# Kernel optimization log

Measured on AMD Instinct MI355X. Metric: run time of the kernel, lower is better.

## Reference

```python
import jax, jax.numpy as jnp
import numpy as np
import math

B, S, HID = 2, 2048, 1536
H, HD = 12, 128           # num_heads, head_dim
LAT = HID // 8            # latent_dim = 192
ROT = HD // 2             # 64, rotary applied to this half-size subspace


def _make_rotary(seq_len, dim=ROT, base=10000.0):
    # LlamaRotaryEmbedding: inv_freq over dim/2 freqs, emb = cat(sin, cos) -> [1,1,S,dim]
    inv_freq = 1.0 / (base ** (np.arange(0, dim, 2, dtype=np.float32) / dim))
    pos = np.arange(seq_len, dtype=np.float32)
    sincos = np.einsum('i,j->ij', pos, inv_freq)  # [S, dim/2]
    emb = np.concatenate([np.sin(sincos), np.cos(sincos)], axis=-1)  # [S, dim]
    return jnp.asarray(emb)[None, None, :, :]


def setup_inputs() -> dict:
    key = jax.random.key(0)
    ks = jax.random.split(key, 10)
    sd = 0.02
    return {
        'hidden_states': jax.random.normal(ks[0], (B, S, HID), jnp.float32),
        'rotary_emb': _make_rotary(S),
        'W_kv_d':  jax.random.normal(ks[1], (HID, LAT), jnp.float32) * sd,
        'W_q_d':   jax.random.normal(ks[2], (HID, LAT), jnp.float32) * sd,
        'W_k_u':   jax.random.normal(ks[3], (LAT, H * ROT), jnp.float32) * sd,
        'W_q_u':   jax.random.normal(ks[4], (LAT, H * ROT), jnp.float32) * sd,
        'W_v_u':   jax.random.normal(ks[5], (LAT, H * HD), jnp.float32) * sd,
        'W_rope_k': jax.random.normal(ks[6], (HID, HID // 2), jnp.float32) * sd,
        'W_rope_q': jax.random.normal(ks[7], (LAT, HID // 2), jnp.float32) * sd,
        'W_o':     jax.random.normal(ks[8], (HID, HID), jnp.float32) * sd,
    }


def _apply_rope(x, emb):
    # x: [B,S,H,ROT]; emb: [1,1,S,ROT] (cat of sin,cos, each ROT/2)
    half = ROT // 2
    x1, x2 = x[..., :half], x[..., half:]
    sin = emb[..., :half].transpose(0, 2, 1, 3)  # -> [1,S,1,half] to broadcast over heads
    cos = emb[..., half:].transpose(0, 2, 1, 3)
    return jnp.concatenate([x1 * cos - x2 * sin, x1 * sin + x2 * cos], axis=-1)


def reference(hidden_states, rotary_emb, W_kv_d, W_q_d, W_k_u, W_q_u, W_v_u,
              W_rope_k, W_rope_q, W_o):
    b, s, _ = hidden_states.shape
    kv_d = hidden_states @ W_kv_d                       # [B,S,LAT]
    q_d = hidden_states @ W_q_d                         # [B,S,LAT]
    k_c = (kv_d @ W_k_u).reshape(b, s, H, ROT)          # content half of K
    q_c = (q_d @ W_q_u).reshape(b, s, H, ROT)
    v = (kv_d @ W_v_u).reshape(b, s, H, HD)
    k_r = (hidden_states @ W_rope_k).reshape(b, s, H, ROT)
    q_r = (q_d @ W_rope_q).reshape(b, s, H, ROT)
    k_r = _apply_rope(k_r, rotary_emb)
    q_r = _apply_rope(q_r, rotary_emb)
    k = jnp.concatenate([k_c, k_r], axis=-1)            # [B,S,H,HD]
    q = jnp.concatenate([q_c, q_r], axis=-1)

    scores = jnp.einsum('bqhd,bkhd->bhqk', q, k) / math.sqrt(HD)
    causal = jnp.tril(jnp.ones((s, s), dtype=bool))
    scores = jnp.where(causal[None, None], scores, jnp.float32(-1e9))
    probs = jax.nn.softmax(scores, axis=-1)
    attn = jnp.einsum('bhqk,bkhd->bqhd', probs, v).reshape(b, s, HID)
    return attn @ W_o
```

## Files before the change

### kernel.cpp

```cpp
#include <hip/hip_runtime.h>
#include <hip/hip_bf16.h>

#define B_ 2
#define S_ 2048
#define HID_ 1536
#define H_ 12
#define HD_ 128
#define LAT_ 192
#define ROT_ 64
#define M_ (B_*S_)
#define NTILE_ (B_*H_*(S_/64))

#define SC2F 0.12752869f

typedef __hip_bfloat16 bf16;

using short8  = __attribute__((ext_vector_type(8))) short;
using short4v = __attribute__((ext_vector_type(4))) short;
using float4v = __attribute__((ext_vector_type(4))) float;

__device__ __forceinline__ unsigned short f2bf(float f) {
  __hip_bfloat16 h = __float2bfloat16(f);
  unsigned short u; __builtin_memcpy(&u, &h, 2); return u;
}

#define GLDS16(gp, lp) __builtin_amdgcn_global_load_lds( \
    (__attribute__((address_space(1))) void*)(size_t)(gp), \
    (__attribute__((address_space(3))) void*)(lp), 16, 0, 0)

__global__ __launch_bounds__(256)
void fillf_k(float* __restrict__ out, float v, int n)
{
  int i = blockIdx.x*256 + threadIdx.x;
  if (i < n) out[i] = v;
}

__global__ __launch_bounds__(256)
void packT5_k(const float* __restrict__ s0, const float* __restrict__ s1,
              const float* __restrict__ s2, const float* __restrict__ s3,
              bf16* __restrict__ d0, bf16* __restrict__ d1,
              bf16* __restrict__ d2, bf16* __restrict__ d3,
              int Kn, int N0, int N1, int N2, int N3,
              const float* __restrict__ hsrc, bf16* __restrict__ hdst)
{
  if (blockIdx.z == 4) {
    const int nblk = gridDim.x * gridDim.y;
    const int flatb = blockIdx.y * gridDim.x + blockIdx.x;
    const float4* in4 = (const float4*)hsrc;
    for (int i = flatb*256 + threadIdx.x; i < M_*HID_/4; i += nblk*256) {
      float4 v = in4[i];
      short4v o;
      o[0] = (short)f2bf(v.x); o[1] = (short)f2bf(v.y);
      o[2] = (short)f2bf(v.z); o[3] = (short)f2bf(v.w);
      *(short4v*)&hdst[i*4] = o;
    }
    return;
  }
  const float* W; bf16* Wt; int Nn;
  switch (blockIdx.z) {
    case 0:  W = s0; Wt = d0; Nn = N0; break;
    case 1:  W = s1; Wt = d1; Nn = N1; break;
    case 2:  W = s2; Wt = d2; Nn = N2; break;
    default: W = s3; Wt = d3; Nn = N3; break;
  }
  const int kb = blockIdx.x*32, nb = blockIdx.y*32;
  if (nb >= Nn) return;
  __shared__ float t[32][33];
  const int tx = threadIdx.x & 31, ty = threadIdx.x >> 5;
  #pragma unroll
  for (int i = 0; i < 4; i++)
    t[ty+8*i][tx] = W[(size_t)(kb+ty+8*i)*Nn + nb + tx];
  __syncthreads();
  #pragma unroll
  for (int i = 0; i < 4; i++)
    Wt[(size_t)(nb + ty + 8*i)*Kn + kb + tx] = __float2bfloat16(t[tx][ty+8*i]);
}

template<int CMODE, int BM>
__global__ __launch_bounds__(256)
void gemm_mfma(const bf16* __restrict__ Av, const bf16* __restrict__ Btp,
               const bf16* __restrict__ Av2, const bf16* __restrict__ Bt2,
               void* __restrict__ Cv, void* __restrict__ Cv2,
               void* __restrict__ Cv3,
               const float* __restrict__ emb, int Kn, int lda, int ldb, int ldc)
{
  constexpr int MI  = BM/32;
  constexpr int ITA = BM/32;
  __shared__ bf16 As[(size_t)BM*64];
  __shared__ bf16 Bs[128*64];

  const int tid  = threadIdx.x;
  const int lane = tid & 63;
  const int w    = tid >> 6;
  const int col  = lane & 15, quad = lane >> 4;
  const int wr   = w >> 1, wc = w & 1;
  const size_t m0 = (size_t)blockIdx.y * BM;
  const size_t n0 = (size_t)blockIdx.x * 128;

  const bf16* Abase = Av;
  const bf16* Bt    = Btp;
  size_t nrow0 = n0;
  if constexpr (CMODE == 6) {
    if ((int)n0 >= 2304) { Abase = Av2; Bt = Bt2; nrow0 = n0 - 2304; }
  }

  const bf16* bg[4];
  #pragma unroll
  for (int it = 0; it < 4; it++) {
    int c = tid + it*256, row = c >> 3, seg = c & 7;
    bg[it] = Bt + (nrow0 + row)*ldb + (size_t)((seg ^ (row & 7))*8);
  }
  const bf16* ag[ITA];
  #pragma unroll
  for (int it = 0; it < ITA; it++) {
    int c = tid + it*256, row = c >> 3, seg = c & 7;
    ag[it] = Abase + (m0 + row)*lda + (size_t)((seg ^ (row & 7))*8);
  }

  float4v acc[MI][4];
  #pragma unroll
  for (int i=0;i<MI;i++)
    #pragma unroll
    for (int j=0;j<4;j++) acc[i][j] = (float4v){0.f,0.f,0.f,0.f};

  for (int k0 = 0; k0 < Kn; k0 += 64) {
    #pragma unroll
    for (int it = 0; it < 4; it++)
      GLDS16(bg[it] + k0, Bs + (size_t)(tid + it*256)*8);
    #pragma unroll
    for (int it = 0; it < ITA; it++)
      GLDS16(ag[it] + k0, As + (size_t)(tid + it*256)*8);
    __syncthreads();

    short8 af[MI][2], bfr[4][2];
    #pragma unroll
    for (int i=0;i<MI;i++) {
      const int ar = wr*(BM/2) + i*16 + col;
      #pragma unroll
      for (int k2=0;k2<2;k2++)
        af[i][k2] = *(const short8*)&As[ar*64 + ((k2*4+quad)^(ar&7))*8];
    }
    #pragma unroll
    for (int j=0;j<4;j++) {
      const int br = wc*64 + j*16 + col;
      #pragma unroll
      for (int k2=0;k2<2;k2++)
        bfr[j][k2] = *(const short8*)&Bs[br*64 + ((k2*4+quad)^(br&7))*8];
    }

    #pragma unroll
    for (int k2=0;k2<2;k2++)
      #pragma unroll
      for (int i=0;i<MI;i++)
        #pragma unroll
        for (int j=0;j<4;j++)
          acc[i][j] = __builtin_amdgcn_mfma_f32_16x16x32_bf16(af[i][k2], bfr[j][k2], acc[i][j], 0,0,0);
    __syncthreads();
  }

  if constexpr (CMODE == 0) {
    #pragma unroll
    for (int i=0;i<MI;i++) {
      const size_t row0 = m0 + wr*(BM/2) + i*16 + quad*4;
      #pragma unroll
      for (int j=0;j<4;j++) {
        const int c = (int)n0 + wc*64 + j*16 + col;
        #pragma unroll
        for (int r=0;r<4;r++)
          ((float*)Cv)[(row0+r)*ldc + c] = acc[i][j][r];
      }
    }
    return;
  }

  if constexpr (CMODE == 5) {
    if ((int)n0 < 384) {
      #pragma unroll
      for (int i=0;i<MI;i++) {
        const size_t row0 = m0 + wr*(BM/2) + i*16 + quad*4;
        #pragma unroll
        for (int j=0;j<4;j++) {
          const int c = (int)n0 + wc*64 + j*16 + col;
          #pragma unroll
          for (int r=0;r<4;r++)
            ((bf16*)Cv)[(row0+r)*384 + c] = __float2bfloat16(acc[i][j][r]);
        }
      }
    } else {
      const int hh = (((int)n0 - 384) >> 6) + wc;
      #pragma unroll
      for (int i=0;i<MI;i++) {
        const size_t row0 = m0 + wr*(BM/2) + i*16 + quad*4;
        #pragma unroll
        for (int j=0;j<2;j++) {
          const int idim = j*16 + col;
          #pragma unroll
          for (int r=0;r<4;r++) {
            const size_t row = row0 + r;
            const int s = (int)(row & (S_-1));
            const float sn = emb[(size_t)s*ROT_ + idim];
            const float cs = emb[(size_t)s*ROT_ + 32 + idim];
            const float x1 = acc[i][j][r], x2 = acc[i][j+2][r];
            bf16* dst = (bf16*)Cv2 + (row*H_ + hh)*HD_ + 64 + idim;
            dst[0]  = __float2bfloat16(x1*cs - x2*sn);
            dst[32] = __float2bfloat16(x1*sn + x2*cs);
          }
        }
      }
    }
    return;
  }

  if ((int)n0 < 768) {
    #pragma unroll
    for (int i=0;i<MI;i++) {
      const size_t row0 = m0 + wr*(BM/2) + i*16 + quad*4;
      #pragma unroll
      for (int j=0;j<4;j++) {
        const int c = (int)n0 + wc*64 + j*16 + col;
        #pragma unroll
        for (int r=0;r<4;r++)
          ((bf16*)Cv)[(row0+r)*HID_ + (c>>6)*HD_ + (c&63)] = __float2bfloat16(acc[i][j][r]);
      }
    }
  } else if ((int)n0 < 2304) {
    #pragma unroll
    for (int i=0;i<MI;i++) {
      const size_t row0 = m0 + wr*(BM/2) + i*16 + quad*4;
      const int bb = (int)(row0 >> 11), s = (int)(row0 & (S_-1));
      #pragma unroll
      for (int j=0;j<4;j++) {
        const int cv = (int)n0 - 768 + wc*64 + j*16 + col;
        const int hh = cv >> 7, d = cv & 127;
        short4v st;
        #pragma unroll
        for (int r=0;r<4;r++) st[r] = (short)f2bf(acc[i][j][r]);
        *(short4v*)((unsigned short*)Cv2 +
            ((size_t)(bb*H_+hh)*HD_ + d)*S_ + s) = st;
      }
    }
  } else if ((int)n0 < 3072) {
    #pragma unroll
    for (int i=0;i<MI;i++) {
      const size_t row0 = m0 + wr*(BM/2) + i*16 + quad*4;
      #pragma unroll
      for (int j=0;j<4;j++) {
        const int c = (int)n0 - 2304 + wc*64 + j*16 + col;
        #pragma unroll
        for (int r=0;r<4;r++)
          ((bf16*)Cv3)[(row0+r)*HID_ + (c>>6)*HD_ + (c&63)] =
              __float2bfloat16(acc[i][j][r] * SC2F);
      }
    }
  } else {
    const int hh = (((int)n0 - 3072) >> 6) + wc;
    #pragma unroll
    for (int i=0;i<MI;i++) {
      const size_t row0 = m0 + wr*(BM/2) + i*16 + quad*4;
      #pragma unroll
      for (int j=0;j<2;j++) {
        const int idim = j*16 + col;
        #pragma unroll
        for (int r=0;r<4;r++) {
          const size_t row = row0 + r;
          const int s = (int)(row & (S_-1));
          const float sn = emb[(size_t)s*ROT_ + idim];
          const float cs = emb[(size_t)s*ROT_ + 32 + idim];
          const float x1 = acc[i][j][r], x2 = acc[i][j+2][r];
          bf16* dst = (bf16*)Cv3 + (row*H_ + hh)*HD_ + 64 + idim;
          dst[0]  = __float2bfloat16((x1*cs - x2*sn) * SC2F);
          dst[32] = __float2bfloat16((x1*sn + x2*cs) * SC2F);
        }
      }
    }
  }
}

#define KSTR 136
#define VSTR 72
#define PSTR 72

__global__ __launch_bounds__(256)
void attn_mfma(const bf16* __restrict__ Qf, const bf16* __restrict__ Kf,
               const bf16* __restrict__ Vtg, bf16* __restrict__ at)
{
  const int rank = (int)blockIdx.x;
  const int qt = (S_/64 - 1) - rank/24;
  const int bh = rank % 24;
  const int h  = bh % H_, b = bh / H_;

  const int tid  = threadIdx.x;
  const int w    = tid >> 6;
  const int lane = tid & 63;
  const int col  = lane & 15;
  const int quad = lane >> 4;

  __shared__ unsigned short Ks[64*KSTR];
  __shared__ unsigned short Vt[128*VSTR];
  __shared__ unsigned short Ps[4][16*PSTR];

  const int q0w = qt*64 + w*16;

  const unsigned short* Kb = (const unsigned short*)Kf +
      ((size_t)b*S_*H_ + h)*HD_;
  const unsigned short* Vb = (const unsigned short*)Vtg +
      (size_t)(b*H_ + h)*HD_*S_;

  const unsigned short* kgp[4]; unsigned short* kdst[4];
  const unsigned short* vgp[4]; unsigned short* vdst[4];
  #pragma unroll
  for (int it = 0; it < 4; it++) {
    int c = tid + it*256;
    int key = c >> 4, doff = (c & 15)*8;
    kgp[it]  = Kb + (size_t)key*HID_ + doff;
    kdst[it] = &Ks[key*KSTR + doff];
    int d = c >> 3, kg = (c & 7)*8;
    vgp[it]  = Vb + (size_t)d*S_ + kg;
    vdst[it] = &Vt[d*VSTR + kg];
  }

  short8 qf[4];
  {
    const unsigned short* qrow = (const unsigned short*)Qf +
        ((size_t)((size_t)b*S_ + q0w + col)*H_ + h)*HD_;
    #pragma unroll
    for (int kk = 0; kk < 4; kk++)
      qf[kk] = *(const short8*)(qrow + kk*32 + quad*8);
  }

  float4v O[8];
  #pragma unroll
  for (int t=0;t<8;t++) O[t] = (float4v){0.f,0.f,0.f,0.f};
  float m_ln = -1e30f, l_ln = 0.f;

  short8 kr[4], vr[4];
  #pragma unroll
  for (int it = 0; it < 4; it++) {
    kr[it] = *(const short8*)kgp[it];
    vr[it] = *(const short8*)vgp[it];
  }

  for (int kb = 0; kb <= qt; kb++) {
    const int k0 = kb * 64;
    const bool diag = (kb == qt);

    #pragma unroll
    for (int it = 0; it < 4; it++) *(short8*)kdst[it] = kr[it];
    #pragma unroll
    for (int it = 0; it < 4; it++) *(short8*)vdst[it] = vr[it];
    __syncthreads();

    if (!diag) {
      const size_t kn = (size_t)(k0 + 64);
      #pragma unroll
      for (int it = 0; it < 4; it++) {
        kr[it] = *(const short8*)(kgp[it] + kn*HID_);
        vr[it] = *(const short8*)(vgp[it] + kn);
      }
    }

    float4v Sf[4];
    #pragma unroll
    for (int tc=0;tc<4;tc++) Sf[tc] = (float4v){0.f,0.f,0.f,0.f};
    __builtin_amdgcn_s_setprio(1);
    if (!diag) {
      #pragma unroll
      for (int tc = 0; tc < 4; tc++)
        #pragma unroll
        for (int kk = 0; kk < 4; kk++) {
          short8 kfrag = *(const short8*)&Ks[(16*tc+col)*KSTR + 32*kk + quad*8];
          Sf[tc] = __builtin_amdgcn_mfma_f32_16x16x32_bf16(kfrag, qf[kk], Sf[tc], 0,0,0);
        }
    } else {
      #pragma unroll
      for (int tc = 0; tc < 4; tc++) {
        if (tc <= w) {
          #pragma unroll
          for (int kk = 0; kk < 4; kk++) {
            short8 kfrag = *(const short8*)&Ks[(16*tc+col)*KSTR + 32*kk + quad*8];
            Sf[tc] = __builtin_amdgcn_mfma_f32_16x16x32_bf16(kfrag, qf[kk], Sf[tc], 0,0,0);
          }
        }
      }
    }
    __builtin_amdgcn_s_setprio(0);

    float sv[4][4];
    if (!diag) {
      #pragma unroll
      for (int tc = 0; tc < 4; tc++)
        #pragma unroll
        for (int r = 0; r < 4; r++)
          sv[tc][r] = Sf[tc][r];
    } else {
      const int qrel = w*16 + col;
      #pragma unroll
      for (int tc = 0; tc < 4; tc++)
        #pragma unroll
        for (int r = 0; r < 4; r++)
          sv[tc][r] = (tc*16 + quad*4 + r > qrel) ? -3.0e38f : Sf[tc][r];
    }
    float ma[4];
    #pragma unroll
    for (int tc = 0; tc < 4; tc++)
      ma[tc] = fmaxf(fmaxf(sv[tc][0], sv[tc][1]), fmaxf(sv[tc][2], sv[tc][3]));
    float pmax = fmaxf(fmaxf(ma[0], ma[1]), fmaxf(ma[2], ma[3]));
    pmax = fmaxf(pmax, __shfl_xor(pmax, 16));
    pmax = fmaxf(pmax, __shfl_xor(pmax, 32));

    if (__all(pmax <= m_ln + 11.0f)) {
      float sa[4];
      #pragma unroll
      for (int tc = 0; tc < 4; tc++) {
        #pragma unroll
        for (int r = 0; r < 4; r++)
          sv[tc][r] = __builtin_amdgcn_exp2f(sv[tc][r] - m_ln);
        sa[tc] = (sv[tc][0] + sv[tc][1]) + (sv[tc][2] + sv[tc][3]);
      }
      float lt = (sa[0] + sa[1]) + (sa[2] + sa[3]);
      lt += __shfl_xor(lt, 16);
      lt += __shfl_xor(lt, 32);
      l_ln += lt;
    } else {
      const float mnew = fmaxf(m_ln, pmax);
      float sa[4];
      #pragma unroll
      for (int tc = 0; tc < 4; tc++) {
        #pragma unroll
        for (int r = 0; r < 4; r++)
          sv[tc][r] = __builtin_amdgcn_exp2f(sv[tc][r] - mnew);
        sa[tc] = (sv[tc][0] + sv[tc][1]) + (sv[tc][2] + sv[tc][3]);
      }
      float lt = (sa[0] + sa[1]) + (sa[2] + sa[3]);
      lt += __shfl_xor(lt, 16);
      lt += __shfl_xor(lt, 32);
      const float al = __builtin_amdgcn_exp2f(m_ln - mnew);
      l_ln = l_ln * al + lt;
      m_ln = mnew;
      float alr[4];
      #pragma unroll
      for (int r = 0; r < 4; r++) alr[r] = __shfl(al, quad*4 + r);
      #pragma unroll
      for (int t = 0; t < 8; t++)
        #pragma unroll
        for (int r = 0; r < 4; r++) O[t][r] *= alr[r];
    }

    #pragma unroll
    for (int tc = 0; tc < 4; tc++) {
      short4v pw;
      pw[0] = (short)f2bf(sv[tc][0]); pw[1] = (short)f2bf(sv[tc][1]);
      pw[2] = (short)f2bf(sv[tc][2]); pw[3] = (short)f2bf(sv[tc][3]);
      *(short4v*)&Ps[w][col*PSTR + tc*16 + quad*4] = pw;
    }

    __builtin_amdgcn_s_setprio(1);
    if (!diag) {
      #pragma unroll
      for (int ks = 0; ks < 2; ks++) {
        short8 pf = *(const short8*)&Ps[w][col*PSTR + 32*ks + quad*8];
        #pragma unroll
        for (int t = 0; t < 8; t++) {
          short8 vf = *(const short8*)&Vt[(16*t + col)*VSTR + 32*ks + quad*8];
          O[t] = __builtin_amdgcn_mfma_f32_16x16x32_bf16(pf, vf, O[t], 0,0,0);
        }
      }
    } else {
      #pragma unroll
      for (int ks = 0; ks < 2; ks++) {
        if (ks == 0 || w >= 2) {
          short8 pf = *(const short8*)&Ps[w][col*PSTR + 32*ks + quad*8];
          #pragma unroll
          for (int t = 0; t < 8; t++) {
            short8 vf = *(const short8*)&Vt[(16*t + col)*VSTR + 32*ks + quad*8];
            O[t] = __builtin_amdgcn_mfma_f32_16x16x32_bf16(pf, vf, O[t], 0,0,0);
          }
        }
      }
    }
    __builtin_amdgcn_s_setprio(0);
    __syncthreads();
  }

  float lr[4];
  #pragma unroll
  for (int r = 0; r < 4; r++) lr[r] = __shfl(l_ln, quad*4 + r);
  #pragma unroll
  for (int r = 0; r < 4; r++) {
    const float linv = 1.f / lr[r];
    const size_t mq = (size_t)b*S_ + q0w + quad*4 + r;
    bf16* dst = at + mq*HID_ + h*HD_ + col;
    #pragma unroll
    for (int t = 0; t < 8; t++)
      dst[16*t] = __float2bfloat16(O[t][r] * linv);
  }
}

extern "C" void kernel_launch(void* const* d_in, const int* in_sizes, int n_in,
                              void* d_out, int out_size, void* d_ws, size_t ws_size,
                              hipStream_t stream)
{
  float* out = (float*)d_out;

  static const int sz_dict[10] = {6291456,131072,294912,294912,147456,
                                  147456,294912,1179648,147456,2359296};
  int bad = -1;
  if (n_in < 10) bad = 15;
  else {
    for (int i = 0; i < 10; i++)
      if (in_sizes[i] != sz_dict[i]) { bad = i; break; }
  }
  if (bad >= 0) {
    float v = 1.0e6f * (float)(1 + bad);
    if (bad < 10) v += (float)(in_sizes[bad] % 1000000);
    fillf_k<<<(out_size + 255)/256, 256, 0, stream>>>(out, v, out_size);
    return;
  }

  const float* hidden = (const float*)d_in[0];
  const float* emb    = (const float*)d_in[1];
  const float* Wkvd   = (const float*)d_in[2];
  const float* Wqd    = (const float*)d_in[3];
  const float* Wku    = (const float*)d_in[4];
  const float* Wqu    = (const float*)d_in[5];
  const float* Wvu    = (const float*)d_in[6];
  const float* Wrk    = (const float*)d_in[7];
  const float* Wrq    = (const float*)d_in[8];
  const float* Wo     = (const float*)d_in[9];

  char* wp = (char*)d_ws;
  size_t used = 0;
  auto alloc = [&](size_t bytes) -> void* {
    void* p = wp + used;
    used += (bytes + 255) & ~(size_t)255;
    return p;
  };
  bf16*  hb    = (bf16*)alloc((size_t)M_*HID_*2);
  bf16*  dout  = (bf16*)alloc((size_t)M_*384*2);
  bf16*  Kf    = (bf16*)alloc((size_t)M_*HID_*2);
  bf16*  Qf    = (bf16*)alloc((size_t)M_*HID_*2);
  bf16*  Vtg   = (bf16*)alloc((size_t)B_*H_*HD_*S_*2);
  bf16*  at    = (bf16*)alloc((size_t)M_*HID_*2);
  bf16*  WdkrT = (bf16*)alloc((size_t)1152*HID_*2);
  bf16*  WkvuT = (bf16*)alloc((size_t)2304*LAT_*2);
  bf16*  WqurT = (bf16*)alloc((size_t)1536*LAT_*2);
  bf16*  WoT   = (bf16*)alloc((size_t)HID_*HID_*2);

  if (used > ws_size) {
    fillf_k<<<(out_size + 255)/256, 256, 0, stream>>>(out, 5.0e7f, out_size);
    return;
  }

  packT5_k<<<dim3(48,48,5), 256, 0, stream>>>(
      Wkvd, Wqd, Wrk, Wo,
      WdkrT, WdkrT + (size_t)192*HID_, WdkrT + (size_t)384*HID_, WoT,
      HID_, LAT_, LAT_, H_*ROT_, HID_,
      hidden, hb);
  packT5_k<<<dim3(6,48,4), 256, 0, stream>>>(
      Wku, Wvu, Wqu, Wrq,
      WkvuT, WkvuT + (size_t)768*LAT_, WqurT, WqurT + (size_t)768*LAT_,
      LAT_, H_*ROT_, HID_, H_*ROT_, H_*ROT_,
      nullptr, nullptr);

  gemm_mfma<5,64><<<dim3(9, M_/64), 256, 0, stream>>>(
      hb, WdkrT, nullptr, nullptr, dout, Kf, nullptr, emb, HID_, HID_, HID_, 0);
  gemm_mfma<6,128><<<dim3(30, M_/128), 256, 0, stream>>>(
      dout, WkvuT, dout + 192, WqurT, Kf, Vtg, Qf, emb, LAT_, 384, LAT_, 0);

  attn_mfma<<<NTILE_, 256, 0, stream>>>(Qf, Kf, Vtg, at);

  gemm_mfma<0,64><<<dim3(12, M_/64), 256, 0, stream>>>(
      at, WoT, nullptr, nullptr, out, nullptr, nullptr, emb, HID_, HID_, HID_, HID_);
}
```

Before: 235.8 us.

## Fuse fp32-to-bf16 hidden conversion into first GEMM and use 64-wide N tiles

Drops the separate pass that converts hidden_states to bf16. The first projection GEMM now loads fp32 A tiles straight from global memory, converts them in registers and writes them swizzled into LDS. This removes a full read-write round trip of the activation buffer. The GEMM template also gains a BN parameter, and the first and output GEMMs move to 64x64 tiles with one wave per 16-row strip, which doubles their block count. The catch is that the fp32 A path uses synchronous register loads instead of async global-to-LDS copies, and smaller tiles give less MFMA work per LDS read.

Result: slower. 264.2 us (+12.0%).

```diff
diff --git a/kernel.cpp b/kernel.cpp
--- a/kernel.cpp
+++ b/kernel.cpp
@@ -36,26 +36,12 @@
 }
 
 __global__ __launch_bounds__(256)
-void packT5_k(const float* __restrict__ s0, const float* __restrict__ s1,
+void packT4_k(const float* __restrict__ s0, const float* __restrict__ s1,
               const float* __restrict__ s2, const float* __restrict__ s3,
               bf16* __restrict__ d0, bf16* __restrict__ d1,
               bf16* __restrict__ d2, bf16* __restrict__ d3,
-              int Kn, int N0, int N1, int N2, int N3,
-              const float* __restrict__ hsrc, bf16* __restrict__ hdst)
+              int Kn, int N0, int N1, int N2, int N3)
 {
-  if (blockIdx.z == 4) {
-    const int nblk = gridDim.x * gridDim.y;
-    const int flatb = blockIdx.y * gridDim.x + blockIdx.x;
-    const float4* in4 = (const float4*)hsrc;
-    for (int i = flatb*256 + threadIdx.x; i < M_*HID_/4; i += nblk*256) {
-      float4 v = in4[i];
-      short4v o;
-      o[0] = (short)f2bf(v.x); o[1] = (short)f2bf(v.y);
-      o[2] = (short)f2bf(v.z); o[3] = (short)f2bf(v.w);
-      *(short4v*)&hdst[i*4] = o;
-    }
-    return;
-  }
   const float* W; bf16* Wt; int Nn;
   switch (blockIdx.z) {
     case 0:  W = s0; Wt = d0; Nn = N0; break;
@@ -76,7 +62,7 @@
     Wt[(size_t)(nb + ty + 8*i)*Kn + kb + tx] = __float2bfloat16(t[tx][ty+8*i]);
 }
 
-template<int CMODE, int BM>
+template<int CMODE, int BM, int BN, int AF32>
 __global__ __launch_bounds__(256)
 void gemm_mfma(const bf16* __restrict__ Av, const bf16* __restrict__ Btp,
                const bf16* __restrict__ Av2, const bf16* __restrict__ Bt2,
@@ -84,18 +70,22 @@
                void* __restrict__ Cv3,
                const float* __restrict__ emb, int Kn, int lda, int ldb, int ldc)
 {
-  constexpr int MI  = BM/32;
-  constexpr int ITA = BM/32;
+  constexpr int WC   = (BN == 128) ? 2 : 1;
+  constexpr int ROWS = (WC == 2) ? BM/2 : BM/4;
+  constexpr int MI   = ROWS/16;
+  constexpr int ITA  = BM/32;
+  constexpr int ITB  = BN/32;
   __shared__ bf16 As[(size_t)BM*64];
-  __shared__ bf16 Bs[128*64];
+  __shared__ bf16 Bs[(size_t)BN*64];
 
   const int tid  = threadIdx.x;
   const int lane = tid & 63;
   const int w    = tid >> 6;
   const int col  = lane & 15, quad = lane >> 4;
-  const int wr   = w >> 1, wc = w & 1;
+  const int wr   = (WC == 2) ? (w >> 1) : w;
+  const int wc   = (WC == 2) ? (w & 1)  : 0;
   const size_t m0 = (size_t)blockIdx.y * BM;
-  const size_t n0 = (size_t)blockIdx.x * 128;
+  const size_t n0 = (size_t)blockIdx.x * BN;
 
   const bf16* Abase = Av;
   const bf16* Bt    = Btp;
@@ -104,17 +94,25 @@
     if ((int)n0 >= 2304) { Abase = Av2; Bt = Bt2; nrow0 = n0 - 2304; }
   }
 
-  const bf16* bg[4];
-  #pragma unroll
-  for (int it = 0; it < 4; it++) {
+  const bf16* bg[ITB];
+  #pragma unroll
+  for (int it = 0; it < ITB; it++) {
     int c = tid + it*256, row = c >> 3, seg = c & 7;
     bg[it] = Bt + (nrow0 + row)*ldb + (size_t)((seg ^ (row & 7))*8);
   }
   const bf16* ag[ITA];
-  #pragma unroll
-  for (int it = 0; it < ITA; it++) {
-    int c = tid + it*256, row = c >> 3, seg = c & 7;
-    ag[it] = Abase + (m0 + row)*lda + (size_t)((seg ^ (row & 7))*8);
+  const float* asrc = nullptr;
+  int arow = 0;
+  if constexpr (AF32) {
+    arow = tid >> 2;
+    const int aseg = tid & 3;
+    asrc = (const float*)Av + (m0 + arow)*lda + aseg*16;
+  } else {
+    #pragma unroll
+    for (int it = 0; it < ITA; it++) {
+      int c = tid + it*256, row = c >> 3, seg = c & 7;
+      ag[it] = Abase + (m0 + row)*lda + (size_t)((seg ^ (row & 7))*8);
+    }
   }
 
   float4v acc[MI][4];
@@ -125,17 +123,37 @@
 
   for (int k0 = 0; k0 < Kn; k0 += 64) {
     #pragma unroll
-    for (int it = 0; it < 4; it++)
+    for (int it = 0; it < ITB; it++)
       GLDS16(bg[it] + k0, Bs + (size_t)(tid + it*256)*8);
-    #pragma unroll
-    for (int it = 0; it < ITA; it++)
-      GLDS16(ag[it] + k0, As + (size_t)(tid + it*256)*8);
+    if constexpr (AF32) {
+      const int aseg = tid & 3;
+      float4 f0 = *(const float4*)(asrc + k0);
+      float4 f1 = *(const float4*)(asrc + k0 + 4);
+      float4 f2 = *(const float4*)(asrc + k0 + 8);
+      float4 f3 = *(const float4*)(asrc + k0 + 12);
+      short8 h0, h1;
+      h0[0]=(short)f2bf(f0.x); h0[1]=(short)f2bf(f0.y);
+      h0[2]=(short)f2bf(f0.z); h0[3]=(short)f2bf(f0.w);
+      h0[4]=(short)f2bf(f1.x); h0[5]=(short)f2bf(f1.y);
+      h0[6]=(short)f2bf(f1.z); h0[7]=(short)f2bf(f1.w);
+      h1[0]=(short)f2bf(f2.x); h1[1]=(short)f2bf(f2.y);
+      h1[2]=(short)f2bf(f2.z); h1[3]=(short)f2bf(f2.w);
+      h1[4]=(short)f2bf(f3.x); h1[5]=(short)f2bf(f3.y);
+      h1[6]=(short)f2bf(f3.z); h1[7]=(short)f2bf(f3.w);
+      const int sl0 = (aseg*2) ^ (arow & 7), sl1 = (aseg*2+1) ^ (arow & 7);
+      *(short8*)&As[arow*64 + sl0*8] = h0;
+      *(short8*)&As[arow*64 + sl1*8] = h1;
+    } else {
+      #pragma unroll
+      for (int it = 0; it < ITA; it++)
+        GLDS16(ag[it] + k0, As + (size_t)(tid + it*256)*8);
+    }
     __syncthreads();
 
     short8 af[MI][2], bfr[4][2];
     #pragma unroll
     for (int i=0;i<MI;i++) {
-      const int ar = wr*(BM/2) + i*16 + col;
+      const int ar = wr*ROWS + i*16 + col;
       #pragma unroll
       for (int k2=0;k2<2;k2++)
         af[i][k2] = *(const short8*)&As[ar*64 + ((k2*4+quad)^(ar&7))*8];
@@ -161,7 +179,7 @@
   if constexpr (CMODE == 0) {
     #pragma unroll
     for (int i=0;i<MI;i++) {
-      const size_t row0 = m0 + wr*(BM/2) + i*16 + quad*4;
+      const size_t row0 = m0 + wr*ROWS + i*16 + quad*4;
       #pragma unroll
       for (int j=0;j<4;j++) {
         const int c = (int)n0 + wc*64 + j*16 + col;
@@ -177,7 +195,7 @@
     if ((int)n0 < 384) {
       #pragma unroll
       for (int i=0;i<MI;i++) {
-        const size_t row0 = m0 + wr*(BM/2) + i*16 + quad*4;
+        const size_t row0 = m0 + wr*ROWS + i*16 + quad*4;
         #pragma unroll
         for (int j=0;j<4;j++) {
           const int c = (int)n0 + wc*64 + j*16 + col;
@@ -190,7 +208,7 @@
       const int hh = (((int)n0 - 384) >> 6) + wc;
       #pragma unroll
       for (int i=0;i<MI;i++) {
-        const size_t row0 = m0 + wr*(BM/2) + i*16 + quad*4;
+        const size_t row0 = m0 + wr*ROWS + i*16 + quad*4;
         #pragma unroll
         for (int j=0;j<2;j++) {
           const int idim = j*16 + col;
@@ -214,7 +232,7 @@
   if ((int)n0 < 768) {
     #pragma unroll
     for (int i=0;i<MI;i++) {
-      const size_t row0 = m0 + wr*(BM/2) + i*16 + quad*4;
+      const size_t row0 = m0 + wr*ROWS + i*16 + quad*4;
       #pragma unroll
       for (int j=0;j<4;j++) {
         const int c = (int)n0 + wc*64 + j*16 + col;
@@ -226,7 +244,7 @@
   } else if ((int)n0 < 2304) {
     #pragma unroll
     for (int i=0;i<MI;i++) {
-      const size_t row0 = m0 + wr*(BM/2) + i*16 + quad*4;
+      const size_t row0 = m0 + wr*ROWS + i*16 + quad*4;
       const int bb = (int)(row0 >> 11), s = (int)(row0 & (S_-1));
       #pragma unroll
       for (int j=0;j<4;j++) {
@@ -242,7 +260,7 @@
   } else if ((int)n0 < 3072) {
     #pragma unroll
     for (int i=0;i<MI;i++) {
-      const size_t row0 = m0 + wr*(BM/2) + i*16 + quad*4;
+      const size_t row0 = m0 + wr*ROWS + i*16 + quad*4;
       #pragma unroll
       for (int j=0;j<4;j++) {
         const int c = (int)n0 - 2304 + wc*64 + j*16 + col;
@@ -256,7 +274,7 @@
     const int hh = (((int)n0 - 3072) >> 6) + wc;
     #pragma unroll
     for (int i=0;i<MI;i++) {
-      const size_t row0 = m0 + wr*(BM/2) + i*16 + quad*4;
+      const size_t row0 = m0 + wr*ROWS + i*16 + quad*4;
       #pragma unroll
       for (int j=0;j<2;j++) {
         const int idim = j*16 + col;
@@ -535,7 +553,6 @@
     used += (bytes + 255) & ~(size_t)255;
     return p;
   };
-  bf16*  hb    = (bf16*)alloc((size_t)M_*HID_*2);
   bf16*  dout  = (bf16*)alloc((size_t)M_*384*2);
   bf16*  Kf    = (bf16*)alloc((size_t)M_*HID_*2);
   bf16*  Qf    = (bf16*)alloc((size_t)M_*HID_*2);
@@ -551,24 +568,23 @@
     return;
   }
 
-  packT5_k<<<dim3(48,48,5), 256, 0, stream>>>(
+  packT4_k<<<dim3(48,48,4), 256, 0, stream>>>(
       Wkvd, Wqd, Wrk, Wo,
       WdkrT, WdkrT + (size_t)192*HID_, WdkrT + (size_t)384*HID_, WoT,
-      HID_, LAT_, LAT_, H_*ROT_, HID_,
-      hidden, hb);
-  packT5_k<<<dim3(6,48,4), 256, 0, stream>>>(
+      HID_, LAT_, LAT_, H_*ROT_, HID_);
+  packT4_k<<<dim3(6,48,4), 256, 0, stream>>>(
       Wku, Wvu, Wqu, Wrq,
       WkvuT, WkvuT + (size_t)768*LAT_, WqurT, WqurT + (size_t)768*LAT_,
-      LAT_, H_*ROT_, HID_, H_*ROT_, H_*ROT_,
-      nullptr, nullptr);
-
-  gemm_mfma<5,64><<<dim3(9, M_/64), 256, 0, stream>>>(
-      hb, WdkrT, nullptr, nullptr, dout, Kf, nullptr, emb, HID_, HID_, HID_, 0);
-  gemm_mfma<6,128><<<dim3(30, M_/128), 256, 0, stream>>>(
+      LAT_, H_*ROT_, HID_, H_*ROT_, H_*ROT_);
+
+  gemm_mfma<5,64,64,1><<<dim3(18, M_/64), 256, 0, stream>>>(
+      (const bf16*)hidden, WdkrT, nullptr, nullptr, dout, Kf, nullptr, emb,
+      HID_, HID_, HID_, 0);
+  gemm_mfma<6,128,128,0><<<dim3(30, M_/128), 256, 0, stream>>>(
       dout, WkvuT, dout + 192, WqurT, Kf, Vtg, Qf, emb, LAT_, 384, LAT_, 0);
 
   attn_mfma<<<NTILE_, 256, 0, stream>>>(Qf, Kf, Vtg, at);
 
-  gemm_mfma<0,64><<<dim3(12, M_/64), 256, 0, stream>>>(
+  gemm_mfma<0,64,64,0><<<dim3(24, M_/64), 256, 0, stream>>>(
       at, WoT, nullptr, nullptr, out, nullptr, nullptr, emb, HID_, HID_, HID_, HID_);
 }
```
